# Optimization experiments

Hardware: AMD Instinct MI355X
Metric: run time of the kernel (lower is better)

The kernel has to match this reference:

```python
import jax, jax.numpy as jnp
import numpy as np

NEG = jnp.float32(-1e10)

def setup_inputs() -> dict:
    key = jax.random.key(0)
    k1, k2, k3, k4 = jax.random.split(key, 4)
    B, Ns, Nr, D = 64, 512, 256, 1024
    return {
        "span_embeddings": jax.random.normal(k1, (B, Ns, D), dtype=jnp.float32),
        "image_embeddings": jax.random.normal(k2, (B, Nr, D), dtype=jnp.float32),
        "span_mask": jax.random.randint(k3, (B, Ns), 0, 2).astype(jnp.int32),
        "image_mask": jax.random.randint(k4, (B, Nr), 0, 2).astype(jnp.int32),
    }

def reference(span_embeddings, image_embeddings, span_mask, image_mask):
    # pair mask: (B, Ns, Nr) = image_mask[b, None, r] * span_mask[b, s, None]
    mask = (image_mask[:, None, :] * span_mask[:, :, None]).astype(span_embeddings.dtype)
    # QK^T with multiplicative mask, then custom zero->-1e10 masking
    att = jnp.einsum('bsd,brd->bsr', span_embeddings, image_embeddings) * mask
    att = jnp.where(att != 0, att, NEG)
    # spans attend over ROIs
    w_first = jax.nn.softmax(att, axis=-1) * mask
    att_first = jnp.einsum('bsr,brd->bsd', w_first, image_embeddings)
    score = jnp.mean(jnp.square(span_embeddings - att_first))
    # ROIs attend over spans (score_type='both')
    att_t = jnp.swapaxes(att, 1, 2)            # (B, Nr, Ns)
    w_second = jax.nn.softmax(att_t, axis=-1) * jnp.swapaxes(mask, 1, 2)
    att_second = jnp.einsum('brs,bsd->brd', w_second, span_embeddings)
    score = score + jnp.mean(jnp.square(image_embeddings - att_second))
    return score, att_first, att
```

## Files before the change

### kernel.cpp

```cpp
#include <hip/hip_runtime.h>
#include <hip/hip_bf16.h>
#include <math.h>

#define B_  64
#define NS  512
#define NR  256
#define DD  1024
#define NEGV (-1e10f)

typedef __attribute__((ext_vector_type(4))) float f32x4;
typedef __attribute__((ext_vector_type(8))) short bf16x8;

__device__ __forceinline__ unsigned short f2bf(float x) {
    unsigned u = __builtin_bit_cast(unsigned, x);
    unsigned r = u + 0x7FFFu + ((u >> 16) & 1u);
    return (unsigned short)(r >> 16);
}
__device__ __forceinline__ unsigned pk2(float x, float y) {
    unsigned r;
    asm("v_cvt_pk_bf16_f32 %0, %1, %2" : "=v"(r) : "v"(x), "v"(y));
    return r;
}
__device__ __forceinline__ void pk_hilo(float x, float y, unsigned& h, unsigned& l) {
    h = pk2(x, y);
    const float hx = __builtin_bit_cast(float, h << 16);
    const float hy = __builtin_bit_cast(float, h & 0xFFFF0000u);
    l = pk2(x - hx, y - hy);
}
__device__ __forceinline__ void gload16(const void* g, void* l) {
    __builtin_amdgcn_global_load_lds((const __attribute__((address_space(1))) void*)g,
                                     (__attribute__((address_space(3))) void*)l, 16, 0, 0);
}

__global__ __launch_bounds__(64) void zero_ws(double* ws) {
    if (threadIdx.x == 0) { ws[0] = 0.0; ws[1] = 0.0; }
}

__global__ __launch_bounds__(256) void att_mfma(
    const float* __restrict__ span, const float* __restrict__ image,
    const int* __restrict__ smask, const int* __restrict__ imask,
    float* __restrict__ att, float2* __restrict__ rowP, float2* __restrict__ colP,
    int doStats) {
    const int b  = blockIdx.z;
    const int s0 = blockIdx.y * 128;
    const int r0 = blockIdx.x * 128;
    __shared__ unsigned short Ah[128][32], Al[128][32], Bh[128][32], Bl[128][32];
    __shared__ float2 rowLDS[128][2];
    __shared__ float2 colLDS[128][2];
    const int tid  = threadIdx.x;
    const int lane = tid & 63;
    const int w    = tid >> 6;
    const int wso  = (w >> 1) * 64;
    const int wro  = (w & 1) * 64;
    const float* Sp = span  + ((size_t)b * NS + s0) * DD;
    const float* Im = image + ((size_t)b * NR + r0) * DD;

    f32x4 acc[4][4];
    #pragma unroll
    for (int i = 0; i < 4; ++i)
        #pragma unroll
        for (int j = 0; j < 4; ++j) acc[i][j] = (f32x4){0.f, 0.f, 0.f, 0.f};

    const int j8   = tid & 7;
    const int row0 = tid >> 3;
    const int krel = j8 * 4;
    const int fr   = lane & 15;
    const int fq   = lane >> 4;

    for (int k0 = 0; k0 < DD; k0 += 32) {
        #pragma unroll
        for (int p = 0; p < 4; ++p) {
            const int row = row0 + p * 32;
            const int wp  = (((j8 >> 1) ^ (row & 3)) << 3) + ((j8 & 1) << 2);
            const float4 a = *reinterpret_cast<const float4*>(Sp + (size_t)row * DD + k0 + krel);
            const float4 c = *reinterpret_cast<const float4*>(Im + (size_t)row * DD + k0 + krel);
            unsigned h0, l0, h1, l1;
            uint2 u;
            pk_hilo(a.x, a.y, h0, l0); pk_hilo(a.z, a.w, h1, l1);
            u.x = h0; u.y = h1; *reinterpret_cast<uint2*>(&Ah[row][wp]) = u;
            u.x = l0; u.y = l1; *reinterpret_cast<uint2*>(&Al[row][wp]) = u;
            pk_hilo(c.x, c.y, h0, l0); pk_hilo(c.z, c.w, h1, l1);
            u.x = h0; u.y = h1; *reinterpret_cast<uint2*>(&Bh[row][wp]) = u;
            u.x = l0; u.y = l1; *reinterpret_cast<uint2*>(&Bl[row][wp]) = u;
        }
        __syncthreads();
        bf16x8 ah[4], al[4], bh[4], bl[4];
        #pragma unroll
        for (int mf = 0; mf < 4; ++mf) {
            const int ra = wso + mf * 16 + fr;
            const int pa_ = (fq ^ (ra & 3)) << 3;
            ah[mf] = *reinterpret_cast<const bf16x8*>(&Ah[ra][pa_]);
            al[mf] = *reinterpret_cast<const bf16x8*>(&Al[ra][pa_]);
            const int rb = wro + mf * 16 + fr;
            const int pb_ = (fq ^ (rb & 3)) << 3;
            bh[mf] = *reinterpret_cast<const bf16x8*>(&Bh[rb][pb_]);
            bl[mf] = *reinterpret_cast<const bf16x8*>(&Bl[rb][pb_]);
        }
        __builtin_amdgcn_s_setprio(1);
        #pragma unroll
        for (int mf = 0; mf < 4; ++mf)
            #pragma unroll
            for (int nf = 0; nf < 4; ++nf) {
                acc[mf][nf] = __builtin_amdgcn_mfma_f32_16x16x32_bf16(ah[mf], bh[nf], acc[mf][nf], 0, 0, 0);
                acc[mf][nf] = __builtin_amdgcn_mfma_f32_16x16x32_bf16(ah[mf], bl[nf], acc[mf][nf], 0, 0, 0);
                acc[mf][nf] = __builtin_amdgcn_mfma_f32_16x16x32_bf16(al[mf], bh[nf], acc[mf][nf], 0, 0, 0);
            }
        __builtin_amdgcn_s_setprio(0);
        __syncthreads();
    }

    const int fq4 = lane >> 4;
    float imvf[4];
    #pragma unroll
    for (int nf = 0; nf < 4; ++nf) imvf[nf] = (float)imask[b * NR + r0 + wro + nf * 16 + fr];
    float cmax[4] = {-3.4e38f, -3.4e38f, -3.4e38f, -3.4e38f};
    float smv[4][4];
    #pragma unroll
    for (int mf = 0; mf < 4; ++mf) {
        #pragma unroll
        for (int i = 0; i < 4; ++i) {
            const int s = s0 + wso + mf * 16 + fq4 * 4 + i;
            const float sv = (float)smask[b * NS + s];
            smv[mf][i] = sv;
            float* orow = att + ((size_t)b * NS + s) * NR + r0 + wro;
            float vj[4];
            #pragma unroll
            for (int nf = 0; nf < 4; ++nf) {
                float v = acc[mf][nf][i] * (sv * imvf[nf]);
                v = (v != 0.0f) ? v : NEGV;
                orow[nf * 16 + fr] = v;
                vj[nf] = v;
                cmax[nf] = fmaxf(cmax[nf], v);
            }
            if (doStats) {
                float rm = fmaxf(fmaxf(vj[0], vj[1]), fmaxf(vj[2], vj[3]));
                rm = fmaxf(rm, __shfl_xor(rm, 1));
                rm = fmaxf(rm, __shfl_xor(rm, 2));
                rm = fmaxf(rm, __shfl_xor(rm, 4));
                rm = fmaxf(rm, __shfl_xor(rm, 8));
                float rs = expf(vj[0] - rm) + expf(vj[1] - rm) + expf(vj[2] - rm) + expf(vj[3] - rm);
                rs += __shfl_xor(rs, 1);
                rs += __shfl_xor(rs, 2);
                rs += __shfl_xor(rs, 4);
                rs += __shfl_xor(rs, 8);
                if (fr == 0) rowLDS[wso + mf * 16 + fq4 * 4 + i][w & 1] = make_float2(rm, rs);
            }
        }
    }
    if (doStats) {
        #pragma unroll
        for (int nf = 0; nf < 4; ++nf) {
            cmax[nf] = fmaxf(cmax[nf], __shfl_xor(cmax[nf], 16));
            cmax[nf] = fmaxf(cmax[nf], __shfl_xor(cmax[nf], 32));
        }
        float csum[4] = {0.f, 0.f, 0.f, 0.f};
        #pragma unroll
        for (int mf = 0; mf < 4; ++mf)
            #pragma unroll
            for (int i = 0; i < 4; ++i)
                #pragma unroll
                for (int nf = 0; nf < 4; ++nf) {
                    float v = acc[mf][nf][i] * (smv[mf][i] * imvf[nf]);
                    v = (v != 0.0f) ? v : NEGV;
                    csum[nf] += expf(v - cmax[nf]);
                }
        #pragma unroll
        for (int nf = 0; nf < 4; ++nf) {
            csum[nf] += __shfl_xor(csum[nf], 16);
            csum[nf] += __shfl_xor(csum[nf], 32);
        }
        if (lane < 16) {
            #pragma unroll
            for (int nf = 0; nf < 4; ++nf)
                colLDS[wro + nf * 16 + lane][w >> 1] = make_float2(cmax[nf], csum[nf]);
        }
        __syncthreads();
        if (tid < 128) {
            const float2 q0 = rowLDS[tid][0], q1 = rowLDS[tid][1];
            const float m = fmaxf(q0.x, q1.x);
            const float ssum = q0.y * expf(q0.x - m) + q1.y * expf(q1.x - m);
            rowP[((size_t)b * NS + s0 + tid) * 2 + blockIdx.x] = make_float2(m, ssum);
        } else {
            const int c = tid - 128;
            const float2 q0 = colLDS[c][0], q1 = colLDS[c][1];
            const float m = fmaxf(q0.x, q1.x);
            const float ssum = q0.y * expf(q0.x - m) + q1.y * expf(q1.x - m);
            colP[((size_t)b * NR + r0 + c) * 4 + blockIdx.y] = make_float2(m, ssum);
        }
    }
}

__global__ __launch_bounds__(256) void combine_stats(
    const float2* __restrict__ rowP, const float2* __restrict__ colP,
    const int* __restrict__ smask, const int* __restrict__ imask,
    float* __restrict__ m1, float* __restrict__ f1,
    float* __restrict__ m2, float* __restrict__ f2) {
    const int idx = blockIdx.x * 256 + threadIdx.x;
    if (idx < B_ * NS) {
        const float2 p0 = rowP[(size_t)idx * 2 + 0];
        const float2 p1 = rowP[(size_t)idx * 2 + 1];
        const float m = fmaxf(p0.x, p1.x);
        const float s = p0.y * expf(p0.x - m) + p1.y * expf(p1.x - m);
        m1[idx] = m;
        f1[idx] = (float)smask[idx] / s;
    } else if (idx < B_ * NS + B_ * NR) {
        const int j = idx - B_ * NS;
        const float2 p0 = colP[(size_t)j * 4 + 0];
        const float2 p1 = colP[(size_t)j * 4 + 1];
        const float2 p2 = colP[(size_t)j * 4 + 2];
        const float2 p3 = colP[(size_t)j * 4 + 3];
        const float m = fmaxf(fmaxf(p0.x, p1.x), fmaxf(p2.x, p3.x));
        const float s = p0.y * expf(p0.x - m) + p1.y * expf(p1.x - m)
                      + p2.y * expf(p2.x - m) + p3.y * expf(p3.x - m);
        m2[j] = m;
        f2[j] = (float)imask[j] / s;
    }
}

__global__ __launch_bounds__(256) void transpose_swz(
    const float* __restrict__ src, unsigned short* __restrict__ dst, int N) {
    const int b = blockIdx.z, n0 = blockIdx.y * 32, d0 = blockIdx.x * 32;
    __shared__ unsigned short T[32][36];
    const int t = threadIdx.x;
    {
        const int n = t >> 3, dq = (t & 7) * 4;
        const float4 v = *reinterpret_cast<const float4*>(src + ((size_t)b * N + n0 + n) * DD + d0 + dq);
        T[dq + 0][n] = f2bf(v.x); T[dq + 1][n] = f2bf(v.y);
        T[dq + 2][n] = f2bf(v.z); T[dq + 3][n] = f2bf(v.w);
    }
    __syncthreads();
    {
        const int d = t >> 3, nq = (t & 7) * 4;
        const int dg = d0 + d;
        const int base = n0 + nq;
        const int pos = (base & 63) ^ ((dg & 7) << 3);
        const size_t idx = ((size_t)b * DD + dg) * N + (base & ~63) + pos;
        *reinterpret_cast<ushort4*>(dst + idx) = *reinterpret_cast<const ushort4*>(&T[d][nq]);
    }
}

__global__ __launch_bounds__(256) void build_w12(
    const float* __restrict__ att, const int* __restrict__ smask,
    const int* __restrict__ imask,
    const float* __restrict__ m1, const float* __restrict__ f1,
    const float* __restrict__ m2, const float* __restrict__ f2,
    unsigned short* __restrict__ w1g, unsigned short* __restrict__ w2g) {
    const int b = blockIdx.z, s0 = blockIdx.y * 64, r0 = blockIdx.x * 64;
    __shared__ unsigned short T[64][68];
    __shared__ float m2s[64], f2s[64], ims[64];
    const int tid = threadIdx.x;
    if (tid < 64) {
        m2s[tid] = m2[b * NR + r0 + tid];
        f2s[tid] = f2[b * NR + r0 + tid];
        ims[tid] = (float)imask[b * NR + r0 + tid];
    }
    __syncthreads();
    {
        const int srow = tid >> 2, rg = (tid & 3) * 16;
        const int s = s0 + srow;
        const float m1v = m1[b * NS + s], f1v = f1[b * NS + s];
        const float smv = (float)smask[b * NS + s];
        const float* arow = att + ((size_t)b * NS + s) * NR + r0;
        const int w1swz = (s & 7) << 3;
        unsigned short* w1row = w1g + ((size_t)b * NS + s) * NR + r0;
        #pragma unroll
        for (int g = 0; g < 4; ++g) {
            const int rr = rg + g * 4;
            const float4 a = *reinterpret_cast<const float4*>(arow + rr);
            const float e0 = expf(a.x - m1v) * f1v * ims[rr + 0];
            const float e1 = expf(a.y - m1v) * f1v * ims[rr + 1];
            const float e2 = expf(a.z - m1v) * f1v * ims[rr + 2];
            const float e3 = expf(a.w - m1v) * f1v * ims[rr + 3];
            uint2 u; u.x = pk2(e0, e1); u.y = pk2(e2, e3);
            *reinterpret_cast<uint2*>(w1row + (rr ^ w1swz)) = u;
            const float q0 = expf(a.x - m2s[rr + 0]) * f2s[rr + 0] * smv;
            const float q1 = expf(a.y - m2s[rr + 1]) * f2s[rr + 1] * smv;
            const float q2 = expf(a.z - m2s[rr + 2]) * f2s[rr + 2] * smv;
            const float q3 = expf(a.w - m2s[rr + 3]) * f2s[rr + 3] * smv;
            const unsigned t0 = pk2(q0, q1), t1 = pk2(q2, q3);
            T[rr + 0][srow] = (unsigned short)(t0 & 0xFFFF);
            T[rr + 1][srow] = (unsigned short)(t0 >> 16);
            T[rr + 2][srow] = (unsigned short)(t1 & 0xFFFF);
            T[rr + 3][srow] = (unsigned short)(t1 >> 16);
        }
    }
    __syncthreads();
    {
        const int rl = tid >> 2, sg = (tid & 3) * 16;
        const int w2swz = (rl & 7) << 3;
        unsigned short* w2row = w2g + ((size_t)b * NR + r0 + rl) * NS + s0;
        #pragma unroll
        for (int g = 0; g < 4; ++g) {
            const int ss = sg + g * 4;
            *reinterpret_cast<ushort4*>(w2row + (ss ^ w2swz)) =
                *reinterpret_cast<const ushort4*>(&T[rl][ss]);
        }
    }
}

template<int KTOT, int MT, bool WOUT, int WIDX>
__global__ __launch_bounds__(256) void gemm_apply(
    const unsigned short* __restrict__ Ag, const unsigned short* __restrict__ Btg,
    const float* __restrict__ ref, float* __restrict__ outp, double* __restrict__ wsum) {
    const int b = blockIdx.z, m0 = blockIdx.y * 64, d0 = blockIdx.x * 256;
    __shared__ unsigned short As[64 * 64];
    __shared__ unsigned short Bs[256 * 64];
    __shared__ float redsum[256];
    const int tid = threadIdx.x, lane = tid & 63, w = tid >> 6;
    const int fr = lane & 15, fq = lane >> 4;
    f32x4 acc[4][4];
    #pragma unroll
    for (int i = 0; i < 4; ++i)
        #pragma unroll
        for (int j = 0; j < 4; ++j) acc[i][j] = (f32x4){0.f, 0.f, 0.f, 0.f};

    const int srow = tid >> 3;
    const int scol = (tid & 7) * 16;
    for (int kc = 0; kc < KTOT / 64; ++kc) {
        const char* asrc = (const char*)(Ag + ((size_t)b * MT + m0) * KTOT) + kc * 128 + scol;
        #pragma unroll
        for (int c = 0; c < 2; ++c)
            gload16(asrc + (size_t)(c * 32 + srow) * (KTOT * 2), (char*)As + (c * 256 + tid) * 16);
        const char* bsrc = (const char*)(Btg + ((size_t)b * DD + d0) * KTOT) + kc * 128 + scol;
        #pragma unroll
        for (int c = 0; c < 8; ++c)
            gload16(bsrc + (size_t)(c * 32 + srow) * (KTOT * 2), (char*)Bs + (c * 256 + tid) * 16);
        __syncthreads();
        #pragma unroll
        for (int ks = 0; ks < 2; ++ks) {
            bf16x8 aF[4], bF[4];
            #pragma unroll
            for (int mf = 0; mf < 4; ++mf) {
                const int row = mf * 16 + fr;
                const int pos = (ks * 32 + fq * 8) ^ ((row & 7) << 3);
                aF[mf] = *reinterpret_cast<const bf16x8*>(&As[row * 64 + pos]);
            }
            #pragma unroll
            for (int nf = 0; nf < 4; ++nf) {
                const int row = w * 64 + nf * 16 + fr;
                const int pos = (ks * 32 + fq * 8) ^ ((row & 7) << 3);
                bF[nf] = *reinterpret_cast<const bf16x8*>(&Bs[row * 64 + pos]);
            }
            #pragma unroll
            for (int mf = 0; mf < 4; ++mf)
                #pragma unroll
                for (int nf = 0; nf < 4; ++nf)
                    acc[mf][nf] = __builtin_amdgcn_mfma_f32_16x16x32_bf16(aF[mf], bF[nf], acc[mf][nf], 0, 0, 0);
        }
        __syncthreads();
    }
    float sumsq = 0.0f;
    #pragma unroll
    for (int mf = 0; mf < 4; ++mf) {
        #pragma unroll
        for (int i = 0; i < 4; ++i) {
            const int row = m0 + mf * 16 + fq * 4 + i;
            const size_t base = ((size_t)b * MT + row) * DD + d0 + w * 64;
            #pragma unroll
            for (int nf = 0; nf < 4; ++nf) {
                const float v = acc[mf][nf][i];
                const float rv = ref[base + nf * 16 + fr];
                if constexpr (WOUT) outp[base + nf * 16 + fr] = v;
                const float dx = rv - v;
                sumsq += dx * dx;
            }
        }
    }
    redsum[tid] = sumsq; __syncthreads();
    for (int off = 128; off; off >>= 1) {
        if (tid < off) redsum[tid] += redsum[tid + off];
        __syncthreads();
    }
    if (tid == 0) atomicAdd(wsum + WIDX, (double)redsum[0]);
}

__global__ __launch_bounds__(256) void first_kernel(
    const float* __restrict__ span, const float* __restrict__ image,
    const int* __restrict__ smask, const int* __restrict__ imask,
    const float* __restrict__ att, float* __restrict__ att_first,
    double* __restrict__ ws) {
    const int b  = blockIdx.y;
    const int s0 = blockIdx.x * 32;
    __shared__ float wT[256][36];
    __shared__ float Is[32][132];
    __shared__ float red[256];
    const int tid  = threadIdx.x;
    const int lane = tid & 63, wave = tid >> 6;
    for (int i = 0; i < 8; ++i) {
        const int srel = wave * 8 + i;
        const int s    = s0 + srel;
        const float4 v = *reinterpret_cast<const float4*>(att + ((size_t)b * NS + s) * NR + lane * 4);
        float m = fmaxf(fmaxf(v.x, v.y), fmaxf(v.z, v.w));
        #pragma unroll
        for (int off = 32; off; off >>= 1) m = fmaxf(m, __shfl_xor(m, off));
        float4 e;
        e.x = expf(v.x - m); e.y = expf(v.y - m); e.z = expf(v.z - m); e.w = expf(v.w - m);
        float sum = e.x + e.y + e.z + e.w;
        #pragma unroll
        for (int off = 32; off; off >>= 1) sum += __shfl_xor(sum, off);
        const float fac = (float)smask[b * NS + s] / sum;
        const int4 im4 = *reinterpret_cast<const int4*>(imask + b * NR + lane * 4);
        wT[lane * 4 + 0][srel] = e.x * fac * (float)im4.x;
        wT[lane * 4 + 1][srel] = e.y * fac * (float)im4.y;
        wT[lane * 4 + 2][srel] = e.z * fac * (float)im4.z;
        wT[lane * 4 + 3][srel] = e.w * fac * (float)im4.w;
    }
    __syncthreads();
    float sumsq = 0.0f;
    const int txd = tid & 31;
    const int tys = tid >> 5;
    const float* Ib = image + (size_t)b * NR * DD;
    for (int dc = 0; dc < 8; ++dc) {
        const int d0 = dc * 128;
        float acc[4][4] = {};
        for (int rc = 0; rc < 8; ++rc) {
            const int r0 = rc * 32;
            {
                const int rr = tid >> 3;
                const int cb = tid & 7;
                const float* src = Ib + (size_t)(r0 + rr) * DD + d0;
                #pragma unroll
                for (int q = 0; q < 4; ++q)
                    *reinterpret_cast<float4*>(&Is[rr][(cb + 8 * q) * 4]) =
                        *reinterpret_cast<const float4*>(src + (cb + 8 * q) * 4);
            }
            __syncthreads();
            #pragma unroll 4
            for (int rr = 0; rr < 32; ++rr) {
                const float4 wv = *reinterpret_cast<const float4*>(&wT[r0 + rr][tys * 4]);
                const float4 iv = *reinterpret_cast<const float4*>(&Is[rr][txd * 4]);
                const float wvv[4] = {wv.x, wv.y, wv.z, wv.w};
                const float ivv[4] = {iv.x, iv.y, iv.z, iv.w};
                #pragma unroll
                for (int i = 0; i < 4; ++i)
                    #pragma unroll
                    for (int j = 0; j < 4; ++j)
                        acc[i][j] += wvv[i] * ivv[j];
            }
            __syncthreads();
        }
        #pragma unroll
        for (int i = 0; i < 4; ++i) {
            const int s = s0 + tys * 4 + i;
            const size_t base = ((size_t)b * NS + s) * DD + d0 + txd * 4;
            const float4 af = {acc[i][0], acc[i][1], acc[i][2], acc[i][3]};
            *reinterpret_cast<float4*>(att_first + base) = af;
            const float4 sp = *reinterpret_cast<const float4*>(span + base);
            float dx;
            dx = sp.x - af.x; sumsq += dx * dx;
            dx = sp.y - af.y; sumsq += dx * dx;
            dx = sp.z - af.z; sumsq += dx * dx;
            dx = sp.w - af.w; sumsq += dx * dx;
        }
    }
    red[tid] = sumsq; __syncthreads();
    for (int off = 128; off; off >>= 1) {
        if (tid < off) red[tid] += red[tid + off];
        __syncthreads();
    }
    if (tid == 0) atomicAdd(ws, (double)red[0]);
}

__global__ __launch_bounds__(256) void second_kernel(
    const float* __restrict__ span, const float* __restrict__ image,
    const int* __restrict__ smask, const int* __restrict__ imask,
    const float* __restrict__ att, double* __restrict__ ws) {
    const int b  = blockIdx.y;
    const int r0 = blockIdx.x * 32;
    __shared__ float w2s[32][36];
    __shared__ float Ss[32][132];
    __shared__ float mArr[32], fArr[32];
    __shared__ float redm[8][32];
    __shared__ float red[256];
    const int tid = threadIdx.x;
    const int rr = tid & 31, q = tid >> 5;
    const float* attb = att + (size_t)b * NS * NR + r0 + rr;
    float mloc = -3.4e38f;
    for (int t = 0; t < 64; ++t)
        mloc = fmaxf(mloc, attb[(size_t)(q * 64 + t) * NR]);
    redm[q][rr] = mloc;
    __syncthreads();
    if (tid < 32) {
        float m = redm[0][tid];
        #pragma unroll
        for (int qq = 1; qq < 8; ++qq) m = fmaxf(m, redm[qq][tid]);
        mArr[tid] = m;
    }
    __syncthreads();
    const float mcol = mArr[rr];
    float sloc = 0.0f;
    for (int t = 0; t < 64; ++t)
        sloc += expf(attb[(size_t)(q * 64 + t) * NR] - mcol);
    redm[q][rr] = sloc;
    __syncthreads();
    if (tid < 32) {
        float s = 0.0f;
        #pragma unroll
        for (int qq = 0; qq < 8; ++qq) s += redm[qq][tid];
        fArr[tid] = (float)imask[b * NR + r0 + tid] / s;
    }
    __syncthreads();
    float sumsq = 0.0f;
    const int txd = tid & 31;
    const int tyr = tid >> 5;
    const float* Sb = span + (size_t)b * NS * DD;
    for (int dc = 0; dc < 8; ++dc) {
        const int d0 = dc * 128;
        float acc[4][4] = {};
        for (int sc = 0; sc < 16; ++sc) {
            const int sb0 = sc * 32;
            {
                const int sr = tid >> 3;
                const int cb = tid & 7;
                const float* src = Sb + (size_t)(sb0 + sr) * DD + d0;
                #pragma unroll
                for (int qq = 0; qq < 4; ++qq)
                    *reinterpret_cast<float4*>(&Ss[sr][(cb + 8 * qq) * 4]) =
                        *reinterpret_cast<const float4*>(src + (cb + 8 * qq) * 4);
            }
            {
                const int ss = tid >> 3;
                const int rq = (tid & 7) * 4;
                const int s  = sb0 + ss;
                const float4 v = *reinterpret_cast<const float4*>(att + ((size_t)b * NS + s) * NR + r0 + rq);
                const float smv = (float)smask[b * NS + s];
                float4 wv;
                wv.x = expf(v.x - mArr[rq + 0]) * fArr[rq + 0] * smv;
                wv.y = expf(v.y - mArr[rq + 1]) * fArr[rq + 1] * smv;
                wv.z = expf(v.z - mArr[rq + 2]) * fArr[rq + 2] * smv;
                wv.w = expf(v.w - mArr[rq + 3]) * fArr[rq + 3] * smv;
                *reinterpret_cast<float4*>(&w2s[ss][rq]) = wv;
            }
            __syncthreads();
            #pragma unroll 4
            for (int ss = 0; ss < 32; ++ss) {
                const float4 wv = *reinterpret_cast<const float4*>(&w2s[ss][tyr * 4]);
                const float4 sv = *reinterpret_cast<const float4*>(&Ss[ss][txd * 4]);
                const float wvv[4] = {wv.x, wv.y, wv.z, wv.w};
                const float svv[4] = {sv.x, sv.y, sv.z, sv.w};
                #pragma unroll
                for (int i = 0; i < 4; ++i)
                    #pragma unroll
                    for (int j = 0; j < 4; ++j)
                        acc[i][j] += wvv[i] * svv[j];
            }
            __syncthreads();
        }
        #pragma unroll
        for (int i = 0; i < 4; ++i) {
            const int r = r0 + tyr * 4 + i;
            const float4 iv = *reinterpret_cast<const float4*>(image + ((size_t)b * NR + r) * DD + d0 + txd * 4);
            float dx;
            dx = iv.x - acc[i][0]; sumsq += dx * dx;
            dx = iv.y - acc[i][1]; sumsq += dx * dx;
            dx = iv.z - acc[i][2]; sumsq += dx * dx;
            dx = iv.w - acc[i][3]; sumsq += dx * dx;
        }
    }
    red[tid] = sumsq; __syncthreads();
    for (int off = 128; off; off >>= 1) {
        if (tid < off) red[tid] += red[tid + off];
        __syncthreads();
    }
    if (tid == 0) atomicAdd(ws + 1, (double)red[0]);
}

__global__ __launch_bounds__(64) void score_kernel(const double* __restrict__ ws, float* __restrict__ out) {
    if (threadIdx.x == 0) {
        out[0] = (float)(ws[0] / (double)((size_t)B_ * NS * DD) +
                         ws[1] / (double)((size_t)B_ * NR * DD));
    }
}

extern "C" void kernel_launch(void* const* d_in, const int* in_sizes, int n_in,
                              void* d_out, int out_size, void* d_ws, size_t ws_size,
                              hipStream_t stream) {
    const float* span  = (const float*)d_in[0];
    const float* image = (const float*)d_in[1];
    const int*   smask = (const int*)d_in[2];
    const int*   imask = (const int*)d_in[3];
    float* out       = (float*)d_out;
    float* att_first = out + 1;
    float* att       = out + 1 + (size_t)B_ * NS * DD;

    char* base = (char*)d_ws;
    double* wsum = (double*)base;
    float* m1 = (float*)(base + 512);
    float* f1 = m1 + (size_t)B_ * NS;
    float* m2 = f1 + (size_t)B_ * NS;
    float* f2 = m2 + (size_t)B_ * NR;
    float2* rowP = (float2*)(f2 + (size_t)B_ * NR);
    float2* colP = rowP + (size_t)B_ * NS * 2;
    char* X0 = (char*)(colP + (size_t)B_ * NR * 4);
    unsigned short* imgT = (unsigned short*)X0;
    unsigned short* w1g  = (unsigned short*)(X0 + (size_t)B_ * DD * NR * 2);
    unsigned short* spT  = (unsigned short*)X0;
    unsigned short* w2g  = (unsigned short*)(X0 + (size_t)B_ * DD * NS * 2);
    const size_t NEED = (size_t)(X0 - base) + (size_t)B_ * DD * NS * 2 + (size_t)B_ * NS * NR * 2;
    const int wsok = (ws_size >= NEED) ? 1 : 0;

    zero_ws<<<dim3(1), dim3(64), 0, stream>>>(wsum);
    att_mfma<<<dim3(NR / 128, NS / 128, B_), dim3(256), 0, stream>>>(
        span, image, smask, imask, att, rowP, colP, wsok);

    if (wsok) {
        combine_stats<<<dim3((B_ * NS + B_ * NR) / 256), dim3(256), 0, stream>>>(
            rowP, colP, smask, imask, m1, f1, m2, f2);
        transpose_swz<<<dim3(DD / 32, NR / 32, B_), dim3(256), 0, stream>>>(image, imgT, NR);
        build_w12<<<dim3(NR / 64, NS / 64, B_), dim3(256), 0, stream>>>(
            att, smask, imask, m1, f1, m2, f2, w1g, w2g);
        gemm_apply<NR, NS, true, 0><<<dim3(DD / 256, NS / 64, B_), dim3(256), 0, stream>>>(
            w1g, imgT, span, att_first, wsum);
        transpose_swz<<<dim3(DD / 32, NS / 32, B_), dim3(256), 0, stream>>>(span, spT, NS);
        gemm_apply<NS, NR, false, 1><<<dim3(DD / 256, NR / 64, B_), dim3(256), 0, stream>>>(
            w2g, spT, image, nullptr, wsum);
    } else {
        first_kernel<<<dim3(NS / 32, B_), dim3(256), 0, stream>>>(span, image, smask, imask, att, att_first, wsum);
        second_kernel<<<dim3(NR / 32, B_), dim3(256), 0, stream>>>(span, image, smask, imask, att, wsum);
    }
    score_kernel<<<dim3(1), dim3(64), 0, stream>>>(wsum, out);
}
```

Before: 309.2 us.

## Double-buffer the QK GEMM main loop and remap blocks to a 1D grid

```diff
diff --git a/kernel.cpp b/kernel.cpp
--- a/kernel.cpp
+++ b/kernel.cpp
@@ -41,12 +41,14 @@
     const int* __restrict__ smask, const int* __restrict__ imask,
     float* __restrict__ att, float2* __restrict__ rowP, float2* __restrict__ colP,
     int doStats) {
-    const int b  = blockIdx.z;
-    const int s0 = blockIdx.y * 128;
-    const int r0 = blockIdx.x * 128;
-    __shared__ unsigned short Ah[128][32], Al[128][32], Bh[128][32], Bl[128][32];
-    __shared__ float2 rowLDS[128][2];
-    __shared__ float2 colLDS[128][2];
+    const int id   = blockIdx.x;
+    const int xr   = id >> 8;
+    const int rest = id & 255;
+    const int ys   = rest & 3;
+    const int b    = rest >> 2;
+    const int s0 = ys * 128;
+    const int r0 = xr * 128;
+    __shared__ unsigned short Ah[2][128][32], Al[2][128][32], Bh[2][128][32], Bl[2][128][32];
     const int tid  = threadIdx.x;
     const int lane = tid & 63;
     const int w    = tid >> 6;
@@ -61,42 +63,57 @@
         #pragma unroll
         for (int j = 0; j < 4; ++j) acc[i][j] = (f32x4){0.f, 0.f, 0.f, 0.f};
 
-    const int j8   = tid & 7;
-    const int row0 = tid >> 3;
-    const int krel = j8 * 4;
-    const int fr   = lane & 15;
-    const int fq   = lane >> 4;
-
-    for (int k0 = 0; k0 < DD; k0 += 32) {
-        #pragma unroll
-        for (int p = 0; p < 4; ++p) {
-            const int row = row0 + p * 32;
-            const int wp  = (((j8 >> 1) ^ (row & 3)) << 3) + ((j8 & 1) << 2);
-            const float4 a = *reinterpret_cast<const float4*>(Sp + (size_t)row * DD + k0 + krel);
-            const float4 c = *reinterpret_cast<const float4*>(Im + (size_t)row * DD + k0 + krel);
-            unsigned h0, l0, h1, l1;
-            uint2 u;
-            pk_hilo(a.x, a.y, h0, l0); pk_hilo(a.z, a.w, h1, l1);
-            u.x = h0; u.y = h1; *reinterpret_cast<uint2*>(&Ah[row][wp]) = u;
-            u.x = l0; u.y = l1; *reinterpret_cast<uint2*>(&Al[row][wp]) = u;
-            pk_hilo(c.x, c.y, h0, l0); pk_hilo(c.z, c.w, h1, l1);
-            u.x = h0; u.y = h1; *reinterpret_cast<uint2*>(&Bh[row][wp]) = u;
-            u.x = l0; u.y = l1; *reinterpret_cast<uint2*>(&Bl[row][wp]) = u;
-        }
-        __syncthreads();
+    const int rws = tid >> 2;
+    const int j4  = tid & 3;
+    const int kq  = j4 * 8;
+    const int fr  = lane & 15;
+    const int fq  = lane >> 4;
+
+    float4 la0[4], lb0[4], la1[4], lb1[4];
+
+    auto LOADB = [&](int k0, float4* la, float4* lb) {
+        la[0] = *reinterpret_cast<const float4*>(Sp + (size_t)rws * DD + k0 + kq);
+        la[1] = *reinterpret_cast<const float4*>(Sp + (size_t)rws * DD + k0 + kq + 4);
+        la[2] = *reinterpret_cast<const float4*>(Sp + (size_t)(rws + 64) * DD + k0 + kq);
+        la[3] = *reinterpret_cast<const float4*>(Sp + (size_t)(rws + 64) * DD + k0 + kq + 4);
+        lb[0] = *reinterpret_cast<const float4*>(Im + (size_t)rws * DD + k0 + kq);
+        lb[1] = *reinterpret_cast<const float4*>(Im + (size_t)rws * DD + k0 + kq + 4);
+        lb[2] = *reinterpret_cast<const float4*>(Im + (size_t)(rws + 64) * DD + k0 + kq);
+        lb[3] = *reinterpret_cast<const float4*>(Im + (size_t)(rws + 64) * DD + k0 + kq + 4);
+    };
+    auto CONVB = [&](const float4* la, const float4* lb, int buf) {
+        #pragma unroll
+        for (int h = 0; h < 2; ++h) {
+            const int r  = rws + h * 64;
+            const int cp = (j4 ^ ((r ^ (r >> 2)) & 3)) << 3;
+            uint4 H, L;
+            pk_hilo(la[2*h].x,   la[2*h].y,   H.x, L.x);
+            pk_hilo(la[2*h].z,   la[2*h].w,   H.y, L.y);
+            pk_hilo(la[2*h+1].x, la[2*h+1].y, H.z, L.z);
+            pk_hilo(la[2*h+1].z, la[2*h+1].w, H.w, L.w);
+            *reinterpret_cast<uint4*>(&Ah[buf][r][cp]) = H;
+            *reinterpret_cast<uint4*>(&Al[buf][r][cp]) = L;
+            pk_hilo(lb[2*h].x,   lb[2*h].y,   H.x, L.x);
+            pk_hilo(lb[2*h].z,   lb[2*h].w,   H.y, L.y);
+            pk_hilo(lb[2*h+1].x, lb[2*h+1].y, H.z, L.z);
+            pk_hilo(lb[2*h+1].z, lb[2*h+1].w, H.w, L.w);
+            *reinterpret_cast<uint4*>(&Bh[buf][r][cp]) = H;
+            *reinterpret_cast<uint4*>(&Bl[buf][r][cp]) = L;
+        }
+    };
+    auto DOMFMA = [&](int buf) {
         bf16x8 ah[4], al[4], bh[4], bl[4];
         #pragma unroll
         for (int mf = 0; mf < 4; ++mf) {
             const int ra = wso + mf * 16 + fr;
-            const int pa_ = (fq ^ (ra & 3)) << 3;
-            ah[mf] = *reinterpret_cast<const bf16x8*>(&Ah[ra][pa_]);
-            al[mf] = *reinterpret_cast<const bf16x8*>(&Al[ra][pa_]);
+            const int ca = (fq ^ ((ra ^ (ra >> 2)) & 3)) << 3;
+            ah[mf] = *reinterpret_cast<const bf16x8*>(&Ah[buf][ra][ca]);
+            al[mf] = *reinterpret_cast<const bf16x8*>(&Al[buf][ra][ca]);
             const int rb = wro + mf * 16 + fr;
-            const int pb_ = (fq ^ (rb & 3)) << 3;
-            bh[mf] = *reinterpret_cast<const bf16x8*>(&Bh[rb][pb_]);
-            bl[mf] = *reinterpret_cast<const bf16x8*>(&Bl[rb][pb_]);
-        }
-        __builtin_amdgcn_s_setprio(1);
+            const int cb = (fq ^ ((rb ^ (rb >> 2)) & 3)) << 3;
+            bh[mf] = *reinterpret_cast<const bf16x8*>(&Bh[buf][rb][cb]);
+            bl[mf] = *reinterpret_cast<const bf16x8*>(&Bl[buf][rb][cb]);
+        }
         #pragma unroll
         for (int mf = 0; mf < 4; ++mf)
             #pragma unroll
@@ -105,10 +122,26 @@
                 acc[mf][nf] = __builtin_amdgcn_mfma_f32_16x16x32_bf16(ah[mf], bl[nf], acc[mf][nf], 0, 0, 0);
                 acc[mf][nf] = __builtin_amdgcn_mfma_f32_16x16x32_bf16(al[mf], bh[nf], acc[mf][nf], 0, 0, 0);
             }
-        __builtin_amdgcn_s_setprio(0);
-        __syncthreads();
-    }
-
+    };
+
+    LOADB(0,  la0, lb0);
+    LOADB(32, la1, lb1);
+    CONVB(la0, lb0, 0);
+    __syncthreads();
+    for (int tt = 0; tt < 16; ++tt) {
+        const int t = tt * 2;
+        if (t + 2 < 32) LOADB((t + 2) * 32, la0, lb0);
+        DOMFMA(0);
+        CONVB(la1, lb1, 1);
+        __syncthreads();
+        if (t + 3 < 32) LOADB((t + 3) * 32, la1, lb1);
+        DOMFMA(1);
+        if (t + 2 < 32) CONVB(la0, lb0, 0);
+        __syncthreads();
+    }
+
+    float2* rowLDS = reinterpret_cast<float2*>(&Ah[0][0][0]);
+    float2* colLDS = reinterpret_cast<float2*>((char*)&Ah[0][0][0] + 2048);
     const int fq4 = lane >> 4;
     float imvf[4];
     #pragma unroll
@@ -138,12 +171,12 @@
                 rm = fmaxf(rm, __shfl_xor(rm, 2));
                 rm = fmaxf(rm, __shfl_xor(rm, 4));
                 rm = fmaxf(rm, __shfl_xor(rm, 8));
-                float rs = expf(vj[0] - rm) + expf(vj[1] - rm) + expf(vj[2] - rm) + expf(vj[3] - rm);
+                float rs = __expf(vj[0] - rm) + __expf(vj[1] - rm) + __expf(vj[2] - rm) + __expf(vj[3] - rm);
                 rs += __shfl_xor(rs, 1);
                 rs += __shfl_xor(rs, 2);
                 rs += __shfl_xor(rs, 4);
                 rs += __shfl_xor(rs, 8);
-                if (fr == 0) rowLDS[wso + mf * 16 + fq4 * 4 + i][w & 1] = make_float2(rm, rs);
+                if (fr == 0) rowLDS[(wso + mf * 16 + fq4 * 4 + i) * 2 + (w & 1)] = make_float2(rm, rs);
             }
         }
     }
@@ -162,7 +195,7 @@
                 for (int nf = 0; nf < 4; ++nf) {
                     float v = acc[mf][nf][i] * (smv[mf][i] * imvf[nf]);
                     v = (v != 0.0f) ? v : NEGV;
-                    csum[nf] += expf(v - cmax[nf]);
+                    csum[nf] += __expf(v - cmax[nf]);
                 }
         #pragma unroll
         for (int nf = 0; nf < 4; ++nf) {
@@ -172,20 +205,20 @@
         if (lane < 16) {
             #pragma unroll
             for (int nf = 0; nf < 4; ++nf)
-                colLDS[wro + nf * 16 + lane][w >> 1] = make_float2(cmax[nf], csum[nf]);
+                colLDS[(wro + nf * 16 + lane) * 2 + (w >> 1)] = make_float2(cmax[nf], csum[nf]);
         }
         __syncthreads();
         if (tid < 128) {
-            const float2 q0 = rowLDS[tid][0], q1 = rowLDS[tid][1];
+            const float2 q0 = rowLDS[tid * 2 + 0], q1 = rowLDS[tid * 2 + 1];
             const float m = fmaxf(q0.x, q1.x);
-            const float ssum = q0.y * expf(q0.x - m) + q1.y * expf(q1.x - m);
-            rowP[((size_t)b * NS + s0 + tid) * 2 + blockIdx.x] = make_float2(m, ssum);
+            const float ssum = q0.y * __expf(q0.x - m) + q1.y * __expf(q1.x - m);
+            rowP[((size_t)b * NS + s0 + tid) * 2 + xr] = make_float2(m, ssum);
         } else {
             const int c = tid - 128;
-            const float2 q0 = colLDS[c][0], q1 = colLDS[c][1];
+            const float2 q0 = colLDS[c * 2 + 0], q1 = colLDS[c * 2 + 1];
             const float m = fmaxf(q0.x, q1.x);
-            const float ssum = q0.y * expf(q0.x - m) + q1.y * expf(q1.x - m);
-            colP[((size_t)b * NR + r0 + c) * 4 + blockIdx.y] = make_float2(m, ssum);
+            const float ssum = q0.y * __expf(q0.x - m) + q1.y * __expf(q1.x - m);
+            colP[((size_t)b * NR + r0 + c) * 4 + ys] = make_float2(m, ssum);
         }
     }
 }
@@ -200,7 +233,7 @@
         const float2 p0 = rowP[(size_t)idx * 2 + 0];
         const float2 p1 = rowP[(size_t)idx * 2 + 1];
         const float m = fmaxf(p0.x, p1.x);
-        const float s = p0.y * expf(p0.x - m) + p1.y * expf(p1.x - m);
+        const float s = p0.y * __expf(p0.x - m) + p1.y * __expf(p1.x - m);
         m1[idx] = m;
         f1[idx] = (float)smask[idx] / s;
     } else if (idx < B_ * NS + B_ * NR) {
@@ -210,8 +243,8 @@
         const float2 p2 = colP[(size_t)j * 4 + 2];
         const float2 p3 = colP[(size_t)j * 4 + 3];
         const float m = fmaxf(fmaxf(p0.x, p1.x), fmaxf(p2.x, p3.x));
-        const float s = p0.y * expf(p0.x - m) + p1.y * expf(p1.x - m)
-                      + p2.y * expf(p2.x - m) + p3.y * expf(p3.x - m);
+        const float s = p0.y * __expf(p0.x - m) + p1.y * __expf(p1.x - m)
+                      + p2.y * __expf(p2.x - m) + p3.y * __expf(p3.x - m);
         m2[j] = m;
         f2[j] = (float)imask[j] / s;
     }
@@ -267,16 +300,16 @@
         for (int g = 0; g < 4; ++g) {
             const int rr = rg + g * 4;
             const float4 a = *reinterpret_cast<const float4*>(arow + rr);
-            const float e0 = expf(a.x - m1v) * f1v * ims[rr + 0];
-            const float e1 = expf(a.y - m1v) * f1v * ims[rr + 1];
-            const float e2 = expf(a.z - m1v) * f1v * ims[rr + 2];
-            const float e3 = expf(a.w - m1v) * f1v * ims[rr + 3];
+            const float e0 = __expf(a.x - m1v) * f1v * ims[rr + 0];
+            const float e1 = __expf(a.y - m1v) * f1v * ims[rr + 1];
+            const float e2 = __expf(a.z - m1v) * f1v * ims[rr + 2];
+            const float e3 = __expf(a.w - m1v) * f1v * ims[rr + 3];
             uint2 u; u.x = pk2(e0, e1); u.y = pk2(e2, e3);
             *reinterpret_cast<uint2*>(w1row + (rr ^ w1swz)) = u;
-            const float q0 = expf(a.x - m2s[rr + 0]) * f2s[rr + 0] * smv;
-            const float q1 = expf(a.y - m2s[rr + 1]) * f2s[rr + 1] * smv;
-            const float q2 = expf(a.z - m2s[rr + 2]) * f2s[rr + 2] * smv;
-            const float q3 = expf(a.w - m2s[rr + 3]) * f2s[rr + 3] * smv;
+            const float q0 = __expf(a.x - m2s[rr + 0]) * f2s[rr + 0] * smv;
+            const float q1 = __expf(a.y - m2s[rr + 1]) * f2s[rr + 1] * smv;
+            const float q2 = __expf(a.z - m2s[rr + 2]) * f2s[rr + 2] * smv;
+            const float q3 = __expf(a.w - m2s[rr + 3]) * f2s[rr + 3] * smv;
             const unsigned t0 = pk2(q0, q1), t1 = pk2(q2, q3);
             T[rr + 0][srow] = (unsigned short)(t0 & 0xFFFF);
             T[rr + 1][srow] = (unsigned short)(t0 >> 16);
@@ -600,7 +633,7 @@
     const int wsok = (ws_size >= NEED) ? 1 : 0;
 
     zero_ws<<<dim3(1), dim3(64), 0, stream>>>(wsum);
-    att_mfma<<<dim3(NR / 128, NS / 128, B_), dim3(256), 0, stream>>>(
+    att_mfma<<<dim3(512), dim3(256), 0, stream>>>(
         span, image, smask, imask, att, rowP, colP, wsok);
 
     if (wsok) {
```

Result: slower. 319.1 us (+3.2%).

## Use 512-thread blocks in QK GEMM with padded LDS and fast exp

Applied to the files above, without the earlier changes.

```diff
diff --git a/kernel.cpp b/kernel.cpp
--- a/kernel.cpp
+++ b/kernel.cpp
@@ -36,7 +36,7 @@
     if (threadIdx.x == 0) { ws[0] = 0.0; ws[1] = 0.0; }
 }
 
-__global__ __launch_bounds__(256) void att_mfma(
+__global__ __launch_bounds__(512) void att_mfma(
     const float* __restrict__ span, const float* __restrict__ image,
     const int* __restrict__ smask, const int* __restrict__ imask,
     float* __restrict__ att, float2* __restrict__ rowP, float2* __restrict__ colP,
@@ -44,147 +44,150 @@
     const int b  = blockIdx.z;
     const int s0 = blockIdx.y * 128;
     const int r0 = blockIdx.x * 128;
-    __shared__ unsigned short Ah[128][32], Al[128][32], Bh[128][32], Bl[128][32];
-    __shared__ float2 rowLDS[128][2];
-    __shared__ float2 colLDS[128][2];
+    __shared__ unsigned short Ah[128][40], Al[128][40], Bh[128][40], Bl[128][40];
     const int tid  = threadIdx.x;
     const int lane = tid & 63;
     const int w    = tid >> 6;
-    const int wso  = (w >> 1) * 64;
-    const int wro  = (w & 1) * 64;
+    const int wso  = (w >> 2) * 64;
+    const int wro  = (w & 3) * 32;
     const float* Sp = span  + ((size_t)b * NS + s0) * DD;
     const float* Im = image + ((size_t)b * NR + r0) * DD;
 
-    f32x4 acc[4][4];
+    f32x4 acc[4][2];
     #pragma unroll
     for (int i = 0; i < 4; ++i)
         #pragma unroll
-        for (int j = 0; j < 4; ++j) acc[i][j] = (f32x4){0.f, 0.f, 0.f, 0.f};
-
-    const int j8   = tid & 7;
-    const int row0 = tid >> 3;
-    const int krel = j8 * 4;
+        for (int j = 0; j < 2; ++j) acc[i][j] = (f32x4){0.f, 0.f, 0.f, 0.f};
+
+    const int row0 = tid >> 2;
+    const int kq   = (tid & 3) * 8;
     const int fr   = lane & 15;
     const int fq   = lane >> 4;
+    const int fk   = fq * 8;
 
     for (int k0 = 0; k0 < DD; k0 += 32) {
-        #pragma unroll
-        for (int p = 0; p < 4; ++p) {
-            const int row = row0 + p * 32;
-            const int wp  = (((j8 >> 1) ^ (row & 3)) << 3) + ((j8 & 1) << 2);
-            const float4 a = *reinterpret_cast<const float4*>(Sp + (size_t)row * DD + k0 + krel);
-            const float4 c = *reinterpret_cast<const float4*>(Im + (size_t)row * DD + k0 + krel);
-            unsigned h0, l0, h1, l1;
-            uint2 u;
-            pk_hilo(a.x, a.y, h0, l0); pk_hilo(a.z, a.w, h1, l1);
-            u.x = h0; u.y = h1; *reinterpret_cast<uint2*>(&Ah[row][wp]) = u;
-            u.x = l0; u.y = l1; *reinterpret_cast<uint2*>(&Al[row][wp]) = u;
-            pk_hilo(c.x, c.y, h0, l0); pk_hilo(c.z, c.w, h1, l1);
-            u.x = h0; u.y = h1; *reinterpret_cast<uint2*>(&Bh[row][wp]) = u;
-            u.x = l0; u.y = l1; *reinterpret_cast<uint2*>(&Bl[row][wp]) = u;
-        }
-        __syncthreads();
-        bf16x8 ah[4], al[4], bh[4], bl[4];
+        {
+            const float4 a0 = *reinterpret_cast<const float4*>(Sp + (size_t)row0 * DD + k0 + kq);
+            const float4 a1 = *reinterpret_cast<const float4*>(Sp + (size_t)row0 * DD + k0 + kq + 4);
+            const float4 c0 = *reinterpret_cast<const float4*>(Im + (size_t)row0 * DD + k0 + kq);
+            const float4 c1 = *reinterpret_cast<const float4*>(Im + (size_t)row0 * DD + k0 + kq + 4);
+            unsigned h0, l0, h1, l1, h2, l2, h3, l3;
+            uint4 u;
+            pk_hilo(a0.x, a0.y, h0, l0); pk_hilo(a0.z, a0.w, h1, l1);
+            pk_hilo(a1.x, a1.y, h2, l2); pk_hilo(a1.z, a1.w, h3, l3);
+            u.x = h0; u.y = h1; u.z = h2; u.w = h3;
+            *reinterpret_cast<uint4*>(&Ah[row0][kq]) = u;
+            u.x = l0; u.y = l1; u.z = l2; u.w = l3;
+            *reinterpret_cast<uint4*>(&Al[row0][kq]) = u;
+            pk_hilo(c0.x, c0.y, h0, l0); pk_hilo(c0.z, c0.w, h1, l1);
+            pk_hilo(c1.x, c1.y, h2, l2); pk_hilo(c1.z, c1.w, h3, l3);
+            u.x = h0; u.y = h1; u.z = h2; u.w = h3;
+            *reinterpret_cast<uint4*>(&Bh[row0][kq]) = u;
+            u.x = l0; u.y = l1; u.z = l2; u.w = l3;
+            *reinterpret_cast<uint4*>(&Bl[row0][kq]) = u;
+        }
+        __syncthreads();
+        bf16x8 ah[4], al[4], bh[2], bl[2];
         #pragma unroll
         for (int mf = 0; mf < 4; ++mf) {
-            const int ra = wso + mf * 16 + fr;
-            const int pa_ = (fq ^ (ra & 3)) << 3;
-            ah[mf] = *reinterpret_cast<const bf16x8*>(&Ah[ra][pa_]);
-            al[mf] = *reinterpret_cast<const bf16x8*>(&Al[ra][pa_]);
-            const int rb = wro + mf * 16 + fr;
-            const int pb_ = (fq ^ (rb & 3)) << 3;
-            bh[mf] = *reinterpret_cast<const bf16x8*>(&Bh[rb][pb_]);
-            bl[mf] = *reinterpret_cast<const bf16x8*>(&Bl[rb][pb_]);
-        }
-        __builtin_amdgcn_s_setprio(1);
+            ah[mf] = *reinterpret_cast<const bf16x8*>(&Ah[wso + mf * 16 + fr][fk]);
+            al[mf] = *reinterpret_cast<const bf16x8*>(&Al[wso + mf * 16 + fr][fk]);
+        }
+        #pragma unroll
+        for (int nf = 0; nf < 2; ++nf) {
+            bh[nf] = *reinterpret_cast<const bf16x8*>(&Bh[wro + nf * 16 + fr][fk]);
+            bl[nf] = *reinterpret_cast<const bf16x8*>(&Bl[wro + nf * 16 + fr][fk]);
+        }
         #pragma unroll
         for (int mf = 0; mf < 4; ++mf)
             #pragma unroll
-            for (int nf = 0; nf < 4; ++nf) {
+            for (int nf = 0; nf < 2; ++nf) {
                 acc[mf][nf] = __builtin_amdgcn_mfma_f32_16x16x32_bf16(ah[mf], bh[nf], acc[mf][nf], 0, 0, 0);
                 acc[mf][nf] = __builtin_amdgcn_mfma_f32_16x16x32_bf16(ah[mf], bl[nf], acc[mf][nf], 0, 0, 0);
                 acc[mf][nf] = __builtin_amdgcn_mfma_f32_16x16x32_bf16(al[mf], bh[nf], acc[mf][nf], 0, 0, 0);
             }
-        __builtin_amdgcn_s_setprio(0);
-        __syncthreads();
-    }
-
-    const int fq4 = lane >> 4;
-    float imvf[4];
+        __syncthreads();
+    }
+
+    float2* rowLDS = reinterpret_cast<float2*>(&Ah[0][0]);
+    float2* colLDS = rowLDS + 512;
+    int imv[2];
     #pragma unroll
-    for (int nf = 0; nf < 4; ++nf) imvf[nf] = (float)imask[b * NR + r0 + wro + nf * 16 + fr];
-    float cmax[4] = {-3.4e38f, -3.4e38f, -3.4e38f, -3.4e38f};
+    for (int nf = 0; nf < 2; ++nf) imv[nf] = imask[b * NR + r0 + wro + nf * 16 + fr];
+    float cmax[2] = {-3.4e38f, -3.4e38f};
     float smv[4][4];
     #pragma unroll
     for (int mf = 0; mf < 4; ++mf) {
         #pragma unroll
         for (int i = 0; i < 4; ++i) {
-            const int s = s0 + wso + mf * 16 + fq4 * 4 + i;
-            const float sv = (float)smask[b * NS + s];
-            smv[mf][i] = sv;
+            const int s = s0 + wso + mf * 16 + fq * 4 + i;
+            const int sm = smask[b * NS + s];
+            smv[mf][i] = (float)sm;
             float* orow = att + ((size_t)b * NS + s) * NR + r0 + wro;
-            float vj[4];
-            #pragma unroll
-            for (int nf = 0; nf < 4; ++nf) {
-                float v = acc[mf][nf][i] * (sv * imvf[nf]);
+            float vj[2];
+            #pragma unroll
+            for (int nf = 0; nf < 2; ++nf) {
+                float v = acc[mf][nf][i] * (float)(sm * imv[nf]);
                 v = (v != 0.0f) ? v : NEGV;
                 orow[nf * 16 + fr] = v;
                 vj[nf] = v;
                 cmax[nf] = fmaxf(cmax[nf], v);
             }
             if (doStats) {
-                float rm = fmaxf(fmaxf(vj[0], vj[1]), fmaxf(vj[2], vj[3]));
+                float rm = fmaxf(vj[0], vj[1]);
                 rm = fmaxf(rm, __shfl_xor(rm, 1));
                 rm = fmaxf(rm, __shfl_xor(rm, 2));
                 rm = fmaxf(rm, __shfl_xor(rm, 4));
                 rm = fmaxf(rm, __shfl_xor(rm, 8));
-                float rs = expf(vj[0] - rm) + expf(vj[1] - rm) + expf(vj[2] - rm) + expf(vj[3] - rm);
+                float rs = __expf(vj[0] - rm) + __expf(vj[1] - rm);
                 rs += __shfl_xor(rs, 1);
                 rs += __shfl_xor(rs, 2);
                 rs += __shfl_xor(rs, 4);
                 rs += __shfl_xor(rs, 8);
-                if (fr == 0) rowLDS[wso + mf * 16 + fq4 * 4 + i][w & 1] = make_float2(rm, rs);
+                if (fr == 0) rowLDS[(wso + mf * 16 + fq * 4 + i) * 4 + (w & 3)] = make_float2(rm, rs);
             }
         }
     }
     if (doStats) {
         #pragma unroll
-        for (int nf = 0; nf < 4; ++nf) {
+        for (int nf = 0; nf < 2; ++nf) {
             cmax[nf] = fmaxf(cmax[nf], __shfl_xor(cmax[nf], 16));
             cmax[nf] = fmaxf(cmax[nf], __shfl_xor(cmax[nf], 32));
         }
-        float csum[4] = {0.f, 0.f, 0.f, 0.f};
+        float csum[2] = {0.f, 0.f};
         #pragma unroll
         for (int mf = 0; mf < 4; ++mf)
             #pragma unroll
             for (int i = 0; i < 4; ++i)
                 #pragma unroll
-                for (int nf = 0; nf < 4; ++nf) {
-                    float v = acc[mf][nf][i] * (smv[mf][i] * imvf[nf]);
+                for (int nf = 0; nf < 2; ++nf) {
+                    float v = acc[mf][nf][i] * (smv[mf][i] * (float)imv[nf]);
                     v = (v != 0.0f) ? v : NEGV;
-                    csum[nf] += expf(v - cmax[nf]);
+                    csum[nf] += __expf(v - cmax[nf]);
                 }
         #pragma unroll
-        for (int nf = 0; nf < 4; ++nf) {
+        for (int nf = 0; nf < 2; ++nf) {
             csum[nf] += __shfl_xor(csum[nf], 16);
             csum[nf] += __shfl_xor(csum[nf], 32);
         }
         if (lane < 16) {
             #pragma unroll
-            for (int nf = 0; nf < 4; ++nf)
-                colLDS[wro + nf * 16 + lane][w >> 1] = make_float2(cmax[nf], csum[nf]);
+            for (int nf = 0; nf < 2; ++nf)
+                colLDS[(wro + nf * 16 + lane) * 2 + (w >> 2)] = make_float2(cmax[nf], csum[nf]);
         }
         __syncthreads();
         if (tid < 128) {
-            const float2 q0 = rowLDS[tid][0], q1 = rowLDS[tid][1];
+            float2 q0 = rowLDS[tid * 4 + 0], q1 = rowLDS[tid * 4 + 1];
+            float2 q2 = rowLDS[tid * 4 + 2], q3 = rowLDS[tid * 4 + 3];
+            const float m = fmaxf(fmaxf(q0.x, q1.x), fmaxf(q2.x, q3.x));
+            const float ssum = q0.y * __expf(q0.x - m) + q1.y * __expf(q1.x - m)
+                             + q2.y * __expf(q2.x - m) + q3.y * __expf(q3.x - m);
+            rowP[((size_t)b * NS + s0 + tid) * 2 + blockIdx.x] = make_float2(m, ssum);
+        } else if (tid < 256) {
+            const int c = tid - 128;
+            const float2 q0 = colLDS[c * 2 + 0], q1 = colLDS[c * 2 + 1];
             const float m = fmaxf(q0.x, q1.x);
-            const float ssum = q0.y * expf(q0.x - m) + q1.y * expf(q1.x - m);
-            rowP[((size_t)b * NS + s0 + tid) * 2 + blockIdx.x] = make_float2(m, ssum);
-        } else {
-            const int c = tid - 128;
-            const float2 q0 = colLDS[c][0], q1 = colLDS[c][1];
-            const float m = fmaxf(q0.x, q1.x);
-            const float ssum = q0.y * expf(q0.x - m) + q1.y * expf(q1.x - m);
+            const float ssum = q0.y * __expf(q0.x - m) + q1.y * __expf(q1.x - m);
             colP[((size_t)b * NR + r0 + c) * 4 + blockIdx.y] = make_float2(m, ssum);
         }
     }
@@ -200,7 +203,7 @@
         const float2 p0 = rowP[(size_t)idx * 2 + 0];
         const float2 p1 = rowP[(size_t)idx * 2 + 1];
         const float m = fmaxf(p0.x, p1.x);
-        const float s = p0.y * expf(p0.x - m) + p1.y * expf(p1.x - m);
+        const float s = p0.y * __expf(p0.x - m) + p1.y * __expf(p1.x - m);
         m1[idx] = m;
         f1[idx] = (float)smask[idx] / s;
     } else if (idx < B_ * NS + B_ * NR) {
@@ -210,8 +213,8 @@
         const float2 p2 = colP[(size_t)j * 4 + 2];
         const float2 p3 = colP[(size_t)j * 4 + 3];
         const float m = fmaxf(fmaxf(p0.x, p1.x), fmaxf(p2.x, p3.x));
-        const float s = p0.y * expf(p0.x - m) + p1.y * expf(p1.x - m)
-                      + p2.y * expf(p2.x - m) + p3.y * expf(p3.x - m);
+        const float s = p0.y * __expf(p0.x - m) + p1.y * __expf(p1.x - m)
+                      + p2.y * __expf(p2.x - m) + p3.y * __expf(p3.x - m);
         m2[j] = m;
         f2[j] = (float)imask[j] / s;
     }
@@ -267,16 +270,16 @@
         for (int g = 0; g < 4; ++g) {
             const int rr = rg + g * 4;
             const float4 a = *reinterpret_cast<const float4*>(arow + rr);
-            const float e0 = expf(a.x - m1v) * f1v * ims[rr + 0];
-            const float e1 = expf(a.y - m1v) * f1v * ims[rr + 1];
-            const float e2 = expf(a.z - m1v) * f1v * ims[rr + 2];
-            const float e3 = expf(a.w - m1v) * f1v * ims[rr + 3];
+            const float e0 = __expf(a.x - m1v) * f1v * ims[rr + 0];
+            const float e1 = __expf(a.y - m1v) * f1v * ims[rr + 1];
+            const float e2 = __expf(a.z - m1v) * f1v * ims[rr + 2];
+            const float e3 = __expf(a.w - m1v) * f1v * ims[rr + 3];
             uint2 u; u.x = pk2(e0, e1); u.y = pk2(e2, e3);
             *reinterpret_cast<uint2*>(w1row + (rr ^ w1swz)) = u;
-            const float q0 = expf(a.x - m2s[rr + 0]) * f2s[rr + 0] * smv;
-            const float q1 = expf(a.y - m2s[rr + 1]) * f2s[rr + 1] * smv;
-            const float q2 = expf(a.z - m2s[rr + 2]) * f2s[rr + 2] * smv;
-            const float q3 = expf(a.w - m2s[rr + 3]) * f2s[rr + 3] * smv;
+            const float q0 = __expf(a.x - m2s[rr + 0]) * f2s[rr + 0] * smv;
+            const float q1 = __expf(a.y - m2s[rr + 1]) * f2s[rr + 1] * smv;
+            const float q2 = __expf(a.z - m2s[rr + 2]) * f2s[rr + 2] * smv;
+            const float q3 = __expf(a.w - m2s[rr + 3]) * f2s[rr + 3] * smv;
             const unsigned t0 = pk2(q0, q1), t1 = pk2(q2, q3);
             T[rr + 0][srow] = (unsigned short)(t0 & 0xFFFF);
             T[rr + 1][srow] = (unsigned short)(t0 >> 16);
@@ -600,7 +603,7 @@
     const int wsok = (ws_size >= NEED) ? 1 : 0;
 
     zero_ws<<<dim3(1), dim3(64), 0, stream>>>(wsum);
-    att_mfma<<<dim3(NR / 128, NS / 128, B_), dim3(256), 0, stream>>>(
+    att_mfma<<<dim3(NR / 128, NS / 128, B_), dim3(512), 0, stream>>>(
         span, image, smask, imask, att, rowP, colP, wsok);
 
     if (wsok) {
```

After: 318.6 us. +3.0%, slower.
